# Optimization experiments

Measured on AMD Instinct MI355X. Metric: run time of the kernel, lower is better.

## Reference

```python
import jax, jax.numpy as jnp
import numpy as np

T = 4096      # tokens
H = 1024      # hidden_size
I = 4096      # intermediate_size
E = 8         # num_experts


def setup_inputs() -> dict:
    key = jax.random.key(0)
    ks = jax.random.split(key, 6)
    s_h = 1.0 / np.sqrt(H)
    s_i = 1.0 / np.sqrt(I)
    return {
        "x":  jax.random.normal(ks[0], (T, H), dtype=jnp.float32),
        "Wg": jax.random.uniform(ks[1], (E, H), jnp.float32, -s_h, s_h),   # gate: Linear(H, E), no bias
        "W1": jax.random.uniform(ks[2], (E, H, I), jnp.float32, -s_h, s_h),
        "b1": jax.random.uniform(ks[3], (E, I), jnp.float32, -s_h, s_h),
        "W2": jax.random.uniform(ks[4], (E, I, H), jnp.float32, -s_i, s_i),
        "b2": jax.random.uniform(ks[5], (E, H), jnp.float32, -s_i, s_i),
    }


def reference(x, Wg, W1, b1, W2, b2):
    # Gate: softmax over experts. gate_scores: [T, E]
    gate_scores = jax.nn.softmax(x @ Wg.T, axis=-1)
    # All experts run densely on all tokens (batched GEMMs).
    h = jax.nn.gelu(jnp.einsum('th,ehi->eti', x, W1) + b1[:, None, :],
                    approximate=False)                      # [E, T, I]
    y = jnp.einsum('eti,eih->eth', h, W2) + b2[:, None, :]  # [E, T, H]
    # Gate-weighted sum over experts (fuses the stack + mul + sum).
    return jnp.einsum('te,eth->th', gate_scores, y)         # [T, H]
```

## Files before the change

### kernel.cpp

```cpp
#include <hip/hip_runtime.h>
#include <math.h>

#define T_TOK 4096
#define H_DIM 1024
#define I_DIM 4096
#define E_NUM 8


typedef short s16x8 __attribute__((ext_vector_type(8)));
typedef float f32x4 __attribute__((ext_vector_type(4)));

__device__ __forceinline__ unsigned short f2b(float f) {
  union { float f; unsigned u; } v; v.f = f;
  unsigned r = v.u + 0x7fffu + ((v.u >> 16) & 1u);
  return (unsigned short)(r >> 16);
}

__device__ __forceinline__ void gld_lds16(short* lds, const short* g) {
  __builtin_amdgcn_global_load_lds(
      (const __attribute__((address_space(1))) void*)g,
      (__attribute__((address_space(3))) void*)lds, 16, 0, 0);
}

__device__ __forceinline__ float gelu_f(float v) {
  float a = fabsf(v);
  float z = a * 0.70710678118f;
  float t = __builtin_amdgcn_rcpf(fmaf(0.47047f, z, 1.0f));
  float p = fmaf(fmaf(0.7478556f, t, -0.0958798f), t, 0.3480242f) * t;
  float e = __expf(-z * z);
  float erf_abs = fmaf(-p, e, 1.0f);
  return fmaf(0.5f * a, erf_abs, 0.5f * v);
}

__global__ __launch_bounds__(256) void gate_kernel(
    const float* __restrict__ x, const float* __restrict__ Wg,
    float* __restrict__ gate)
{
  int t = blockIdx.x * 4 + (threadIdx.x >> 6);
  int lane = threadIdx.x & 63;
  const float* xr = x + (size_t)t * H_DIM;
  float acc[E_NUM];
#pragma unroll
  for (int e = 0; e < E_NUM; ++e) acc[e] = 0.f;
  for (int j = 0; j < H_DIM / 64; ++j) {
    float xv = xr[lane + j * 64];
#pragma unroll
    for (int e = 0; e < E_NUM; ++e)
      acc[e] += xv * Wg[e * H_DIM + lane + j * 64];
  }
#pragma unroll
  for (int e = 0; e < E_NUM; ++e)
    for (int s = 32; s > 0; s >>= 1)
      acc[e] += __shfl_xor(acc[e], s, 64);
  if (lane == 0) {
    float mx = acc[0];
#pragma unroll
    for (int e = 1; e < E_NUM; ++e) mx = fmaxf(mx, acc[e]);
    float sum = 0.f, ex[E_NUM];
#pragma unroll
    for (int e = 0; e < E_NUM; ++e) { ex[e] = expf(acc[e] - mx); sum += ex[e]; }
    float inv = 1.f / sum;
#pragma unroll
    for (int e = 0; e < E_NUM; ++e) gate[t * E_NUM + e] = ex[e] * inv;
  }
}

__global__ __launch_bounds__(256) void convert_x_kernel(
    const float* __restrict__ x, short* __restrict__ xb)
{
  int idx = blockIdx.x * 256 + threadIdx.x;
  int t = idx >> 7;
  int h0 = (idx & 127) << 3;
  const float* src = x + (size_t)t * H_DIM + h0;
  float4 a = *(const float4*)src;
  float4 b = *(const float4*)(src + 4);
  s16x8 v;
  v[0] = f2b(a.x); v[1] = f2b(a.y); v[2] = f2b(a.z); v[3] = f2b(a.w);
  v[4] = f2b(b.x); v[5] = f2b(b.y); v[6] = f2b(b.z); v[7] = f2b(b.w);
  int rb = t >> 8, kt = h0 >> 6, half = (t >> 7) & 1;
  size_t off = ((size_t)((rb * 16 + kt) * 2 + half)) * 8192
             + (size_t)(t & 127) * 64 + (h0 & 63);
  *(s16x8*)(xb + off) = v;
}

__global__ __launch_bounds__(256) void trans_w1_kernel(
    const float* __restrict__ W1, short* __restrict__ W1t)
{
  __shared__ short tile[64][65];
  const int e = blockIdx.z;
  const int i0 = blockIdx.x * 64, h0 = blockIdx.y * 64;
  const int tid = threadIdx.x, c = tid & 63, r0 = tid >> 6;
  const float* src = W1 + ((size_t)e * H_DIM + h0) * I_DIM + i0;
#pragma unroll
  for (int j = 0; j < 16; ++j) {
    int r = j * 4 + r0;
    tile[r][c] = f2b(src[(size_t)r * I_DIM + c]);
  }
  __syncthreads();
  const int i = tid & 63, kq = tid >> 6;
  const size_t base = ((size_t)((e * 16 + (i0 >> 8)) * 16 + (h0 >> 6)) * 2
                       + ((i0 >> 7) & 1)) * 8192
                    + (size_t)((i0 & 64) + i) * 64;
#pragma unroll
  for (int w = 0; w < 2; ++w) {
    int kcl = kq + w * 4;
    s16x8 v;
#pragma unroll
    for (int j = 0; j < 8; ++j) v[j] = tile[kcl * 8 + j][i];
    *(s16x8*)(W1t + base + kcl * 8) = v;
  }
}

__global__ __launch_bounds__(256) void trans_w2_kernel(
    const float* __restrict__ W2, short* __restrict__ W2t)
{
  __shared__ short tile[64][65];
  const int e = blockIdx.z;
  const int i0 = blockIdx.x * 64, h0 = blockIdx.y * 64;
  const int tid = threadIdx.x, c = tid & 63, r0 = tid >> 6;
  const float* src = W2 + ((size_t)e * I_DIM + i0) * H_DIM + h0;
#pragma unroll
  for (int j = 0; j < 16; ++j) {
    int r = j * 4 + r0;
    tile[r][c] = f2b(src[(size_t)r * H_DIM + c]);
  }
  __syncthreads();
  const int h = tid & 63, kq = tid >> 6;
  const size_t base = ((size_t)((h0 >> 8) * 512 + e * 64 + (i0 >> 6)) * 2
                       + ((h0 >> 7) & 1)) * 8192
                    + (size_t)((h0 & 64) + h) * 64;
#pragma unroll
  for (int w = 0; w < 2; ++w) {
    int kcl = kq + w * 4;
    s16x8 v;
#pragma unroll
    for (int j = 0; j < 8; ++j) v[j] = tile[kcl * 8 + j][h];
    *(s16x8*)(W2t + base + kcl * 8) = v;
  }
}


#define BARR()  __builtin_amdgcn_s_barrier()
#define FENCE() asm volatile("" ::: "memory")
#define LGKM0() do { asm volatile("s_waitcnt lgkmcnt(0)" ::: "memory"); \
                     __builtin_amdgcn_sched_barrier(0); } while (0)
#define VMC(N)  asm volatile("s_waitcnt vmcnt(" #N ")" ::: "memory")
#define PRIO1() __builtin_amdgcn_s_setprio(1)
#define PRIO0() __builtin_amdgcn_s_setprio(0)
#define SCHEDB() __builtin_amdgcn_sched_barrier(0)
#define MF(A, B, C) __builtin_amdgcn_mfma_f32_16x16x32_bf16(A, B, C, 0, 0, 0)

__device__ __forceinline__ void gemm_core(
    const short* __restrict__ Ag, const short* __restrict__ Bg,
    int nk, short* lds, f32x4 acc[8][4])
{
  const int tid  = threadIdx.x;
  const int wave = tid >> 6, lane = tid & 63;
  const int wm = wave >> 2, wn = wave & 3;
  const int g = lane >> 4, r16 = lane & 15;

  const int L0 = tid * 16;
  const int L1 = 8192 + tid * 16;
  const int s0 = (L0 ^ (((L0 >> 7) & 7) << 4)) >> 1;
  const int s1 = (L1 ^ (((L1 >> 7) & 7) << 4)) >> 1;

  short* stA = lds + wave * 512;
  short* stB = lds + 32768 + wave * 512;

  const int xr_ = (r16 & 7) << 4;
  const int rd0 = r16 * 64 + ((((0 << 6) | (g << 4)) ^ xr_) >> 1);
  const int rd1 = r16 * 64 + ((((1 << 6) | (g << 4)) ^ xr_) >> 1);

  const short* Ah = lds + wm * 8192;
  const short* Bh = lds + 32768 + (wn >> 1) * 8192 + (wn & 1) * 4096;

  s16x8 bf[8];
  s16x8 a0, a1, a2, a3;

#define STAGE_A(KT, HH, BUF) do { \
    const short* _s = Ag + (size_t)(KT) * 16384 + (HH) * 8192; \
    short* _d = stA + ((BUF) * 2 + (HH)) * 8192; \
    gld_lds16(_d, _s + s0); \
    gld_lds16(_d + 4096, _s + s1); } while (0)
#define STAGE_B(KT, HH, BUF) do { \
    const short* _s = Bg + (size_t)(KT) * 16384 + (HH) * 8192; \
    short* _d = stB + ((BUF) * 2 + (HH)) * 8192; \
    gld_lds16(_d, _s + s0); \
    gld_lds16(_d + 4096, _s + s1); } while (0)
#define LDB_ALL(BUF) \
    _Pragma("unroll") \
    for (int n = 0; n < 4; ++n) { \
      bf[n * 2]     = *(const s16x8*)(Bh + (BUF) * 16384 + n * 1024 + rd0); \
      bf[n * 2 + 1] = *(const s16x8*)(Bh + (BUF) * 16384 + n * 1024 + rd1); }
#define LDA_PAIR(BUF, P) do { \
    a0 = *(const s16x8*)(Ah + (BUF) * 16384 + (2 * (P)) * 1024 + rd0); \
    a1 = *(const s16x8*)(Ah + (BUF) * 16384 + (2 * (P)) * 1024 + rd1); \
    a2 = *(const s16x8*)(Ah + (BUF) * 16384 + (2 * (P) + 1) * 1024 + rd0); \
    a3 = *(const s16x8*)(Ah + (BUF) * 16384 + (2 * (P) + 1) * 1024 + rd1); } while (0)
#define MFMA_PAIR(P) \
    _Pragma("unroll") \
    for (int n = 0; n < 4; ++n) { \
      acc[2 * (P)][n]     = MF(a0, bf[n * 2],     acc[2 * (P)][n]); \
      acc[2 * (P)][n]     = MF(a1, bf[n * 2 + 1], acc[2 * (P)][n]); \
      acc[2 * (P) + 1][n] = MF(a2, bf[n * 2],     acc[2 * (P) + 1][n]); \
      acc[2 * (P) + 1][n] = MF(a3, bf[n * 2 + 1], acc[2 * (P) + 1][n]); }

  STAGE_A(0, 0, 0); STAGE_A(0, 1, 0); STAGE_B(0, 0, 0); STAGE_B(0, 1, 0);
  STAGE_B(1, 0, 1); STAGE_B(1, 1, 1);
  VMC(4);
  BARR(); FENCE();

  const int iters = nk >> 1;
  for (int it = 0; it < iters; ++it) {
    const int u = it * 2, v = u + 1;
    const bool nlast = (it + 1 < iters);

    LDB_ALL(0); LDA_PAIR(0, 0);
    STAGE_A(v, 0, 1);
    BARR(); LGKM0();
    PRIO1(); MFMA_PAIR(0); PRIO0();
    SCHEDB(); BARR(); FENCE();

    LDA_PAIR(0, 1);
    STAGE_A(v, 1, 1);
    BARR(); LGKM0();
    PRIO1(); MFMA_PAIR(1); PRIO0();
    SCHEDB(); BARR(); FENCE();

    LDA_PAIR(0, 2);
    if (nlast) STAGE_B(u + 2, 0, 0);
    BARR(); LGKM0();
    PRIO1(); MFMA_PAIR(2); PRIO0();
    SCHEDB(); BARR(); FENCE();

    LDA_PAIR(0, 3);
    if (nlast) STAGE_B(u + 2, 1, 0);
    BARR(); LGKM0();
    PRIO1(); MFMA_PAIR(3); PRIO0();
    if (nlast) { VMC(4); } else { VMC(0); }
    SCHEDB(); BARR(); FENCE();

    LDB_ALL(1); LDA_PAIR(1, 0);
    if (nlast) STAGE_A(u + 2, 0, 0);
    BARR(); LGKM0();
    PRIO1(); MFMA_PAIR(0); PRIO0();
    SCHEDB(); BARR(); FENCE();

    LDA_PAIR(1, 1);
    if (nlast) STAGE_A(u + 2, 1, 0);
    BARR(); LGKM0();
    PRIO1(); MFMA_PAIR(1); PRIO0();
    SCHEDB(); BARR(); FENCE();

    LDA_PAIR(1, 2);
    if (nlast) STAGE_B(v + 2, 0, 1);
    BARR(); LGKM0();
    PRIO1(); MFMA_PAIR(2); PRIO0();
    SCHEDB(); BARR(); FENCE();

    LDA_PAIR(1, 3);
    if (nlast) STAGE_B(v + 2, 1, 1);
    BARR(); LGKM0();
    PRIO1(); MFMA_PAIR(3); PRIO0();
    if (nlast) VMC(4);
    SCHEDB(); BARR(); FENCE();
  }
#undef STAGE_A
#undef STAGE_B
#undef LDB_ALL
#undef LDA_PAIR
#undef MFMA_PAIR
}

__global__ __launch_bounds__(512) void gemm1_kernel(
    const short* __restrict__ xb, const short* __restrict__ W1t,
    const float* __restrict__ b1, const float* __restrict__ gate,
    short* __restrict__ hg)
{
  extern __shared__ short lds[];
  const int bi = blockIdx.x, bt = blockIdx.y, e = blockIdx.z;
  f32x4 acc[8][4];
#pragma unroll
  for (int i = 0; i < 8; ++i)
#pragma unroll
    for (int j = 0; j < 4; ++j) acc[i][j] = (f32x4){0.f, 0.f, 0.f, 0.f};

  const short* Ag = W1t + (size_t)(e * 16 + bi) * 16 * 16384;
  const short* Bg = xb + (size_t)bt * 16 * 16384;
  gemm_core(Ag, Bg, 16, lds, acc);

  const int tid = threadIdx.x, wave = tid >> 6, lane = tid & 63;
  const int wm = wave >> 2, wn = wave & 3, g = lane >> 4, r16 = lane & 15;
#pragma unroll
  for (int mg = 0; mg < 8; ++mg) {
    const int i4 = bi * 256 + wm * 128 + mg * 16 + g * 4;
    const float4 b1v = *(const float4*)(b1 + e * I_DIM + i4);
    const int kt = (e * I_DIM + i4) >> 6;
    const int c = i4 & 63;
    short* dst = hg + ((size_t)(bt * 512 + kt) * 2 + (wn >> 1)) * 8192 + c;
#pragma unroll
    for (int ng = 0; ng < 4; ++ng) {
      const int tl = wn * 64 + ng * 16 + r16;
      const float gt = gate[(bt * 256 + tl) * E_NUM + e];
      const float v0 = gelu_f(acc[mg][ng][0] + b1v.x) * gt;
      const float v1 = gelu_f(acc[mg][ng][1] + b1v.y) * gt;
      const float v2 = gelu_f(acc[mg][ng][2] + b1v.z) * gt;
      const float v3 = gelu_f(acc[mg][ng][3] + b1v.w) * gt;
      int2 pk;
      pk.x = (int)((unsigned)f2b(v0) | ((unsigned)f2b(v1) << 16));
      pk.y = (int)((unsigned)f2b(v2) | ((unsigned)f2b(v3) << 16));
      *(int2*)(dst + (size_t)(tl & 127) * 64) = pk;
    }
  }
}

__global__ __launch_bounds__(512) void gemm2_kernel(
    const short* __restrict__ W2t, const short* __restrict__ hg,
    float* __restrict__ part)
{
  extern __shared__ short lds[];
  const int bh = blockIdx.x, bt = blockIdx.y, ks = blockIdx.z;
  f32x4 acc[8][4];
#pragma unroll
  for (int i = 0; i < 8; ++i)
#pragma unroll
    for (int j = 0; j < 4; ++j) acc[i][j] = (f32x4){0.f, 0.f, 0.f, 0.f};

  const short* Ag = W2t + (size_t)(bh * 512 + ks * 128) * 16384;
  const short* Bg = hg  + (size_t)(bt * 512 + ks * 128) * 16384;
  gemm_core(Ag, Bg, 128, lds, acc);

  const int tid = threadIdx.x, wave = tid >> 6, lane = tid & 63;
  const int wm = wave >> 2, wn = wave & 3, g = lane >> 4, r16 = lane & 15;
  float* dst = part + (size_t)ks * ((size_t)T_TOK * H_DIM);
#pragma unroll
  for (int mg = 0; mg < 8; ++mg) {
    const int h4 = bh * 256 + wm * 128 + mg * 16 + g * 4;
#pragma unroll
    for (int ng = 0; ng < 4; ++ng) {
      const int t = bt * 256 + wn * 64 + ng * 16 + r16;
      *(f32x4*)(dst + (size_t)t * H_DIM + h4) = acc[mg][ng];
    }
  }
}

__global__ __launch_bounds__(256) void reduce_kernel(
    const float* __restrict__ part, const float* __restrict__ gate,
    const float* __restrict__ b2, float* __restrict__ out)
{
  const int idx = blockIdx.x * 256 + threadIdx.x;
  const int t = idx >> 8;
  const int h4 = (idx & 255) << 2;
  const size_t off = (size_t)t * H_DIM + h4;
  const size_t SL = (size_t)T_TOK * H_DIM;
  float4 a0 = *(const float4*)(part + off);
  float4 a1 = *(const float4*)(part + SL + off);
  float4 a2 = *(const float4*)(part + 2 * SL + off);
  float4 a3 = *(const float4*)(part + 3 * SL + off);
  float sx = a0.x + a1.x + a2.x + a3.x;
  float sy = a0.y + a1.y + a2.y + a3.y;
  float sz = a0.z + a1.z + a2.z + a3.z;
  float sw = a0.w + a1.w + a2.w + a3.w;
#pragma unroll
  for (int e = 0; e < E_NUM; ++e) {
    const float gv = gate[t * E_NUM + e];
    const float4 bv = *(const float4*)(b2 + e * H_DIM + h4);
    sx = fmaf(gv, bv.x, sx); sy = fmaf(gv, bv.y, sy);
    sz = fmaf(gv, bv.z, sz); sw = fmaf(gv, bv.w, sw);
  }
  float4 r; r.x = sx; r.y = sy; r.z = sz; r.w = sw;
  *(float4*)(out + off) = r;
}

extern "C" void kernel_launch(void* const* d_in, const int* in_sizes, int n_in,
                              void* d_out, int out_size, void* d_ws, size_t ws_size,
                              hipStream_t stream) {
  const float* x  = (const float*)d_in[0];
  const float* Wg = (const float*)d_in[1];
  const float* W1 = (const float*)d_in[2];
  const float* b1 = (const float*)d_in[3];
  const float* W2 = (const float*)d_in[4];
  const float* b2 = (const float*)d_in[5];
  float* out = (float*)d_out;

  char* ws = (char*)d_ws;
  float* gate = (float*)ws;
  short* xb   = (short*)(ws + 131072);
  short* W1t  = (short*)(ws + 131072 + 8388608);
  short* W2t  = (short*)(ws + 131072 + 8388608 + 67108864);
  short* hg   = (short*)(ws + 131072 + 8388608 + 2 * 67108864);
  float* part = (float*)(ws + 131072);

  static bool attr_done = false;
  if (!attr_done) {
    hipFuncSetAttribute((const void*)gemm1_kernel,
                        hipFuncAttributeMaxDynamicSharedMemorySize, 131072);
    hipFuncSetAttribute((const void*)gemm2_kernel,
                        hipFuncAttributeMaxDynamicSharedMemorySize, 131072);
    attr_done = true;
  }

  gate_kernel<<<T_TOK / 4, 256, 0, stream>>>(x, Wg, gate);
  convert_x_kernel<<<2048, 256, 0, stream>>>(x, xb);
  trans_w1_kernel<<<dim3(I_DIM / 64, H_DIM / 64, E_NUM), 256, 0, stream>>>(W1, W1t);
  trans_w2_kernel<<<dim3(I_DIM / 64, H_DIM / 64, E_NUM), 256, 0, stream>>>(W2, W2t);
  gemm1_kernel<<<dim3(16, 16, 8), 512, 131072, stream>>>(xb, W1t, b1, gate, hg);
  gemm2_kernel<<<dim3(4, 16, 4), 512, 131072, stream>>>(W2t, hg, part);
  reduce_kernel<<<4096, 256, 0, stream>>>(part, gate, b2, out);
}
```

Measured before the change: 873.0 us.

## Loop experts inside persistent gemm1 block, pipelining loads across expert boundaries

The gemm1 kernel previously launched one block per (i-tile, token-tile, expert). Now each block loops over all 8 experts, with a custom inline pipeline that prefetches the next expert's A/B tiles while the epilogue of the current one runs. This removes per-block prologue and pipeline drain costs and keeps the x tile warm. In exchange the grid shrinks from 2048 to 256 blocks, which may underfill the 256 CUs and serialises the per-expert epilogue inside each block.

```diff
diff --git a/kernel.cpp b/kernel.cpp
--- a/kernel.cpp
+++ b/kernel.cpp
@@ -278,40 +278,158 @@
     short* __restrict__ hg)
 {
   extern __shared__ short lds[];
-  const int bi = blockIdx.x, bt = blockIdx.y, e = blockIdx.z;
+  const int bi = blockIdx.x, bt = blockIdx.y;
+
+  const int tid  = threadIdx.x;
+  const int wave = tid >> 6, lane = tid & 63;
+  const int wm = wave >> 2, wn = wave & 3;
+  const int g = lane >> 4, r16 = lane & 15;
+
+  const int L0 = tid * 16;
+  const int L1 = 8192 + tid * 16;
+  const int s0 = (L0 ^ (((L0 >> 7) & 7) << 4)) >> 1;
+  const int s1 = (L1 ^ (((L1 >> 7) & 7) << 4)) >> 1;
+
+  short* stA = lds + wave * 512;
+  short* stB = lds + 32768 + wave * 512;
+
+  const int xr_ = (r16 & 7) << 4;
+  const int rd0 = r16 * 64 + ((((0 << 6) | (g << 4)) ^ xr_) >> 1);
+  const int rd1 = r16 * 64 + ((((1 << 6) | (g << 4)) ^ xr_) >> 1);
+
+  const short* Ah = lds + wm * 8192;
+  const short* Bh = lds + 32768 + (wn >> 1) * 8192 + (wn & 1) * 4096;
+
+  const short* Aw = W1t + (size_t)bi * 16 * 16384;
+  const short* Bw = xb  + (size_t)bt * 16 * 16384;
+
   f32x4 acc[8][4];
 #pragma unroll
   for (int i = 0; i < 8; ++i)
 #pragma unroll
     for (int j = 0; j < 4; ++j) acc[i][j] = (f32x4){0.f, 0.f, 0.f, 0.f};
 
-  const short* Ag = W1t + (size_t)(e * 16 + bi) * 16 * 16384;
-  const short* Bg = xb + (size_t)bt * 16 * 16384;
-  gemm_core(Ag, Bg, 16, lds, acc);
-
-  const int tid = threadIdx.x, wave = tid >> 6, lane = tid & 63;
-  const int wm = wave >> 2, wn = wave & 3, g = lane >> 4, r16 = lane & 15;
-#pragma unroll
-  for (int mg = 0; mg < 8; ++mg) {
-    const int i4 = bi * 256 + wm * 128 + mg * 16 + g * 4;
-    const float4 b1v = *(const float4*)(b1 + e * I_DIM + i4);
-    const int kt = (e * I_DIM + i4) >> 6;
-    const int c = i4 & 63;
-    short* dst = hg + ((size_t)(bt * 512 + kt) * 2 + (wn >> 1)) * 8192 + c;
-#pragma unroll
-    for (int ng = 0; ng < 4; ++ng) {
-      const int tl = wn * 64 + ng * 16 + r16;
-      const float gt = gate[(bt * 256 + tl) * E_NUM + e];
-      const float v0 = gelu_f(acc[mg][ng][0] + b1v.x) * gt;
-      const float v1 = gelu_f(acc[mg][ng][1] + b1v.y) * gt;
-      const float v2 = gelu_f(acc[mg][ng][2] + b1v.z) * gt;
-      const float v3 = gelu_f(acc[mg][ng][3] + b1v.w) * gt;
-      int2 pk;
-      pk.x = (int)((unsigned)f2b(v0) | ((unsigned)f2b(v1) << 16));
-      pk.y = (int)((unsigned)f2b(v2) | ((unsigned)f2b(v3) << 16));
-      *(int2*)(dst + (size_t)(tl & 127) * 64) = pk;
+  s16x8 bf[8];
+  s16x8 a0, a1, a2, a3;
+
+#define STAGE_A1(KK, HH, BUF) do { \
+    const short* _s = Aw + ((size_t)(((KK) >> 4) * 256 + ((KK) & 15))) * 16384 \
+                    + (HH) * 8192; \
+    short* _d = stA + ((BUF) * 2 + (HH)) * 8192; \
+    gld_lds16(_d, _s + s0); \
+    gld_lds16(_d + 4096, _s + s1); } while (0)
+#define STAGE_B1(KK, HH, BUF) do { \
+    const short* _s = Bw + ((size_t)((KK) & 15)) * 16384 + (HH) * 8192; \
+    short* _d = stB + ((BUF) * 2 + (HH)) * 8192; \
+    gld_lds16(_d, _s + s0); \
+    gld_lds16(_d + 4096, _s + s1); } while (0)
+#define LDB_ALL1(BUF) \
+    _Pragma("unroll") \
+    for (int n = 0; n < 4; ++n) { \
+      bf[n * 2]     = *(const s16x8*)(Bh + (BUF) * 16384 + n * 1024 + rd0); \
+      bf[n * 2 + 1] = *(const s16x8*)(Bh + (BUF) * 16384 + n * 1024 + rd1); }
+#define LDA_PAIR1(BUF, P) do { \
+    a0 = *(const s16x8*)(Ah + (BUF) * 16384 + (2 * (P)) * 1024 + rd0); \
+    a1 = *(const s16x8*)(Ah + (BUF) * 16384 + (2 * (P)) * 1024 + rd1); \
+    a2 = *(const s16x8*)(Ah + (BUF) * 16384 + (2 * (P) + 1) * 1024 + rd0); \
+    a3 = *(const s16x8*)(Ah + (BUF) * 16384 + (2 * (P) + 1) * 1024 + rd1); } while (0)
+#define MFMA_PAIR1(P) \
+    _Pragma("unroll") \
+    for (int n = 0; n < 4; ++n) { \
+      acc[2 * (P)][n]     = MF(a0, bf[n * 2],     acc[2 * (P)][n]); \
+      acc[2 * (P)][n]     = MF(a1, bf[n * 2 + 1], acc[2 * (P)][n]); \
+      acc[2 * (P) + 1][n] = MF(a2, bf[n * 2],     acc[2 * (P) + 1][n]); \
+      acc[2 * (P) + 1][n] = MF(a3, bf[n * 2 + 1], acc[2 * (P) + 1][n]); }
+
+  STAGE_A1(0, 0, 0); STAGE_A1(0, 1, 0); STAGE_B1(0, 0, 0); STAGE_B1(0, 1, 0);
+  STAGE_B1(1, 0, 1); STAGE_B1(1, 1, 1);
+  VMC(4);
+  BARR(); FENCE();
+
+  for (int e = 0; e < E_NUM; ++e) {
+    for (int it8 = 0; it8 < 8; ++it8) {
+      const int u = e * 16 + it8 * 2, v = u + 1;
+      const bool nlast = !(e == E_NUM - 1 && it8 == 7);
+
+      LDB_ALL1(0); LDA_PAIR1(0, 0);
+      STAGE_A1(v, 0, 1);
+      BARR(); LGKM0();
+      PRIO1(); MFMA_PAIR1(0); PRIO0();
+      SCHEDB(); BARR(); FENCE();
+
+      LDA_PAIR1(0, 1);
+      STAGE_A1(v, 1, 1);
+      BARR(); LGKM0();
+      PRIO1(); MFMA_PAIR1(1); PRIO0();
+      SCHEDB(); BARR(); FENCE();
+
+      LDA_PAIR1(0, 2);
+      if (nlast) STAGE_B1(u + 2, 0, 0);
+      BARR(); LGKM0();
+      PRIO1(); MFMA_PAIR1(2); PRIO0();
+      SCHEDB(); BARR(); FENCE();
+
+      LDA_PAIR1(0, 3);
+      if (nlast) STAGE_B1(u + 2, 1, 0);
+      BARR(); LGKM0();
+      PRIO1(); MFMA_PAIR1(3); PRIO0();
+      if (nlast) { VMC(4); } else { VMC(0); }
+      SCHEDB(); BARR(); FENCE();
+
+      LDB_ALL1(1); LDA_PAIR1(1, 0);
+      if (nlast) STAGE_A1(u + 2, 0, 0);
+      BARR(); LGKM0();
+      PRIO1(); MFMA_PAIR1(0); PRIO0();
+      SCHEDB(); BARR(); FENCE();
+
+      LDA_PAIR1(1, 1);
+      if (nlast) STAGE_A1(u + 2, 1, 0);
+      BARR(); LGKM0();
+      PRIO1(); MFMA_PAIR1(1); PRIO0();
+      SCHEDB(); BARR(); FENCE();
+
+      LDA_PAIR1(1, 2);
+      if (nlast) STAGE_B1(v + 2, 0, 1);
+      BARR(); LGKM0();
+      PRIO1(); MFMA_PAIR1(2); PRIO0();
+      SCHEDB(); BARR(); FENCE();
+
+      LDA_PAIR1(1, 3);
+      if (nlast) STAGE_B1(v + 2, 1, 1);
+      BARR(); LGKM0();
+      PRIO1(); MFMA_PAIR1(3); PRIO0();
+      if (nlast) VMC(4);
+      SCHEDB(); BARR(); FENCE();
     }
-  }
+
+#pragma unroll
+    for (int mg = 0; mg < 8; ++mg) {
+      const int i4 = bi * 256 + wm * 128 + mg * 16 + g * 4;
+      const float4 b1v = *(const float4*)(b1 + e * I_DIM + i4);
+      const int kt = (e * I_DIM + i4) >> 6;
+      const int c = i4 & 63;
+      short* dst = hg + ((size_t)(bt * 512 + kt) * 2 + (wn >> 1)) * 8192 + c;
+#pragma unroll
+      for (int ng = 0; ng < 4; ++ng) {
+        const int tl = wn * 64 + ng * 16 + r16;
+        const float gt = gate[(bt * 256 + tl) * E_NUM + e];
+        const float v0 = gelu_f(acc[mg][ng][0] + b1v.x) * gt;
+        const float v1 = gelu_f(acc[mg][ng][1] + b1v.y) * gt;
+        const float v2 = gelu_f(acc[mg][ng][2] + b1v.z) * gt;
+        const float v3 = gelu_f(acc[mg][ng][3] + b1v.w) * gt;
+        int2 pk;
+        pk.x = (int)((unsigned)f2b(v0) | ((unsigned)f2b(v1) << 16));
+        pk.y = (int)((unsigned)f2b(v2) | ((unsigned)f2b(v3) << 16));
+        *(int2*)(dst + (size_t)(tl & 127) * 64) = pk;
+        acc[mg][ng] = (f32x4){0.f, 0.f, 0.f, 0.f};
+      }
+    }
+  }
+#undef STAGE_A1
+#undef STAGE_B1
+#undef LDB_ALL1
+#undef LDA_PAIR1
+#undef MFMA_PAIR1
 }
 
 __global__ __launch_bounds__(512) void gemm2_kernel(
@@ -404,7 +522,7 @@
   convert_x_kernel<<<2048, 256, 0, stream>>>(x, xb);
   trans_w1_kernel<<<dim3(I_DIM / 64, H_DIM / 64, E_NUM), 256, 0, stream>>>(W1, W1t);
   trans_w2_kernel<<<dim3(I_DIM / 64, H_DIM / 64, E_NUM), 256, 0, stream>>>(W2, W2t);
-  gemm1_kernel<<<dim3(16, 16, 8), 512, 131072, stream>>>(xb, W1t, b1, gate, hg);
+  gemm1_kernel<<<dim3(16, 16), 512, 131072, stream>>>(xb, W1t, b1, gate, hg);
   gemm2_kernel<<<dim3(4, 16, 4), 512, 131072, stream>>>(W2t, hg, part);
   reduce_kernel<<<4096, 256, 0, stream>>>(part, gate, b2, out);
 }
```

Result: no change. 883.2 us (+1.2%).
